# Kernel optimization log

Hardware: AMD Instinct MI355X
Metric: run time of the kernel (lower is better)

The kernel has to match this reference:

```python
import jax, jax.numpy as jnp
import numpy as np

B, S, D, H = 8, 1024, 1024, 16
DH = D // H  # per-head dim = 64
SCALE = float(np.sqrt(DH))  # normalize_coeff = sqrt(dim_h_k)


def _ln(x, g, b, eps=1e-5):
    m = jnp.mean(x, axis=-1, keepdims=True)
    v = jnp.mean(jnp.square(x - m), axis=-1, keepdims=True)
    return (x - m) / jnp.sqrt(v + eps) * g + b


def setup_inputs() -> dict:
    key = jax.random.key(0)
    ks = jax.random.split(key, 12)
    w = lambda k, shape: (jax.random.normal(k, shape, dtype=jnp.float32) * 0.02)
    return {
        "X": jax.random.normal(ks[0], (B, S, D), dtype=jnp.float32),
        # stacked per-head projection weights (torch Linear: y = x @ W.T + b -> store as [H, D, DH])
        "Wq": w(ks[1], (H, D, DH)), "bq": jnp.zeros((H, DH), jnp.float32),
        "Wk": w(ks[2], (H, D, DH)), "bk": jnp.zeros((H, DH), jnp.float32),
        "Wv": w(ks[3], (H, D, DH)), "bv": jnp.zeros((H, DH), jnp.float32),
        "pre_g": jnp.ones((D,), jnp.float32), "pre_b": jnp.zeros((D,), jnp.float32),
        "post_g": jnp.ones((D,), jnp.float32), "post_b": jnp.zeros((D,), jnp.float32),
        "W1": w(ks[4], (D, 2 * D)), "b1": jnp.zeros((2 * D,), jnp.float32),
        "ln1_g": jnp.ones((2 * D,), jnp.float32), "ln1_b": jnp.zeros((2 * D,), jnp.float32),
        "W2": w(ks[5], (2 * D, D)), "b2": jnp.zeros((D,), jnp.float32),
        "ln2_g": jnp.ones((D,), jnp.float32), "ln2_b": jnp.zeros((D,), jnp.float32),
    }


def reference(X, Wq, bq, Wk, bk, Wv, bv, pre_g, pre_b, post_g, post_b,
              W1, b1, ln1_g, ln1_b, W2, b2, ln2_g, ln2_b):
    # pre-LN + multi-head attention (all heads batched instead of python loop)
    t = _ln(X, pre_g, pre_b)
    q = jnp.einsum('bsd,hdk->bhsk', t, Wq) + bq[:, None, :]   # [B,H,S,DH]
    k = jnp.einsum('bsd,hdk->bhsk', t, Wk) + bk[:, None, :]
    v = jnp.einsum('bsd,hdk->bhsk', t, Wv) + bv[:, None, :]
    scores = jnp.einsum('bhqd,bhkd->bhqk', q, k) / SCALE       # [B,H,S,S]
    p = jax.nn.softmax(scores, axis=-1)
    o = jnp.einsum('bhqk,bhkd->bhqd', p, v)                    # [B,H,S,DH]
    o = o.transpose(0, 2, 1, 3).reshape(B, S, D)               # concat heads
    X = X + o
    # post-LN + MLP (Linear -> LN -> GELU -> Linear -> LN -> GELU)
    t2 = _ln(X, post_g, post_b)
    h = jax.nn.gelu(_ln(t2 @ W1 + b1, ln1_g, ln1_b), approximate=False)
    h = jax.nn.gelu(_ln(h @ W2 + b2, ln2_g, ln2_b), approximate=False)
    return X + h
```

## Files before the change

### kernel.cpp

```cpp
#include <hip/hip_runtime.h>

typedef __attribute__((ext_vector_type(8))) short s16x8;
typedef __attribute__((ext_vector_type(8))) unsigned short u16x8;
typedef __attribute__((ext_vector_type(4))) unsigned short u16x4;
typedef __attribute__((ext_vector_type(4))) float f32x4;

__device__ __forceinline__ unsigned short f2bf(float f) {
  union { float f; unsigned int u; } v; v.f = f;
  unsigned int r = (v.u + 0x7FFFu + ((v.u >> 16) & 1u)) >> 16;
  return (unsigned short)r;
}
__device__ __forceinline__ float bf2f(unsigned short h) {
  union { unsigned int u; float f; } v; v.u = ((unsigned int)h) << 16;
  return v.f;
}
__device__ __forceinline__ float gelu(float x) {
  return 0.5f * x * (1.f + erff(x * 0.70710678118654752f));
}
__device__ __forceinline__ float fexp2(float x) {
  float r; asm("v_exp_f32 %0, %1" : "=v"(r) : "v"(x)); return r;
}

__device__ __forceinline__ void gld16(const void* g, void* l) {
  __builtin_amdgcn_global_load_lds(
      (const __attribute__((address_space(1))) unsigned int*)g,
      (__attribute__((address_space(3))) unsigned int*)l, 16, 0, 0);
}

__device__ __forceinline__ float blk_sum(float v, float* red, int tid, int nw) {
#pragma unroll
  for (int m = 32; m >= 1; m >>= 1) v += __shfl_xor(v, m);
  __syncthreads();
  if ((tid & 63) == 0) red[tid >> 6] = v;
  __syncthreads();
  float t = 0.f;
  for (int i = 0; i < nw; ++i) t += red[i];
  return t;
}

__global__ __launch_bounds__(256) void k_tr(
    const float* __restrict__ in, unsigned short* __restrict__ out,
    int inRS, int outRS, long inBS, long outBS) {
  __shared__ float t[32][33];
  const float* ip = in + (size_t)blockIdx.z * inBS;
  unsigned short* op = out + (size_t)blockIdx.z * outBS;
  const int r0 = blockIdx.y * 32, c0 = blockIdx.x * 32;
  const int tid = threadIdx.x;
  const int r = tid >> 3, c4 = (tid & 7) * 4;
  const f32x4 v = *(const f32x4*)(ip + (size_t)(r0 + r) * inRS + c0 + c4);
#pragma unroll
  for (int i = 0; i < 4; ++i) t[r][c4 + i] = v[i];
  __syncthreads();
  u16x4 o;
#pragma unroll
  for (int i = 0; i < 4; ++i) o[i] = f2bf(t[c4 + i][r]);
  *(u16x4*)(op + (size_t)(c0 + r) * outRS + r0 + c4) = o;
}

__global__ __launch_bounds__(256) void k_bias3(
    const float* __restrict__ a, const float* __restrict__ b,
    const float* __restrict__ c, float* __restrict__ o) {
  int i = blockIdx.x * 256 + threadIdx.x;
  if (i >= 3072) return;
  o[i] = (i < 1024) ? a[i] : ((i < 2048) ? b[i - 1024] : c[i - 2048]);
}

__global__ __launch_bounds__(256) void k_pre_ln(
    const float* __restrict__ X, const float* __restrict__ g,
    const float* __restrict__ bta, unsigned short* __restrict__ out) {
  __shared__ float red[4];
  const int row = blockIdx.x, tid = threadIdx.x;
  const f32x4 x = *(const f32x4*)(X + (size_t)row * 1024 + tid * 4);
  float s = x[0] + x[1] + x[2] + x[3];
  s = blk_sum(s, red, tid, 4);
  const float mean = s * (1.f / 1024.f);
  f32x4 d;
#pragma unroll
  for (int i = 0; i < 4; ++i) d[i] = x[i] - mean;
  float sq = d[0] * d[0] + d[1] * d[1] + d[2] * d[2] + d[3] * d[3];
  sq = blk_sum(sq, red, tid, 4);
  const float rstd = rsqrtf(sq * (1.f / 1024.f) + 1e-5f);
  const f32x4 gv = *(const f32x4*)(g + tid * 4);
  const f32x4 bv = *(const f32x4*)(bta + tid * 4);
  u16x4 o;
#pragma unroll
  for (int i = 0; i < 4; ++i) o[i] = f2bf(d[i] * rstd * gv[i] + bv[i]);
  *(u16x4*)(out + (size_t)row * 1024 + tid * 4) = o;
}

__global__ __launch_bounds__(256) void k_res_ln(
    const float* __restrict__ X, const unsigned short* __restrict__ attn,
    const float* __restrict__ g, const float* __restrict__ bta,
    float* __restrict__ X1, unsigned short* __restrict__ t2) {
  __shared__ float red[4];
  const int row = blockIdx.x, tid = threadIdx.x;
  const f32x4 x = *(const f32x4*)(X + (size_t)row * 1024 + tid * 4);
  const u16x4 a = *(const u16x4*)(attn + (size_t)row * 1024 + tid * 4);
  f32x4 x1;
#pragma unroll
  for (int i = 0; i < 4; ++i) x1[i] = x[i] + bf2f(a[i]);
  *(f32x4*)(X1 + (size_t)row * 1024 + tid * 4) = x1;
  float s = x1[0] + x1[1] + x1[2] + x1[3];
  s = blk_sum(s, red, tid, 4);
  const float mean = s * (1.f / 1024.f);
  f32x4 d;
#pragma unroll
  for (int i = 0; i < 4; ++i) d[i] = x1[i] - mean;
  float sq = d[0] * d[0] + d[1] * d[1] + d[2] * d[2] + d[3] * d[3];
  sq = blk_sum(sq, red, tid, 4);
  const float rstd = rsqrtf(sq * (1.f / 1024.f) + 1e-5f);
  const f32x4 gv = *(const f32x4*)(g + tid * 4);
  const f32x4 bv = *(const f32x4*)(bta + tid * 4);
  u16x4 o;
#pragma unroll
  for (int i = 0; i < 4; ++i) o[i] = f2bf(d[i] * rstd * gv[i] + bv[i]);
  *(u16x4*)(t2 + (size_t)row * 1024 + tid * 4) = o;
}

__global__ __launch_bounds__(256) void k_ln_gelu(
    const unsigned short* __restrict__ in, const float* __restrict__ g,
    const float* __restrict__ bta, unsigned short* __restrict__ out) {
  __shared__ float red[4];
  const int row = blockIdx.x, tid = threadIdx.x;
  const u16x8 iv = *(const u16x8*)(in + (size_t)row * 2048 + tid * 8);
  float v[8];
  float s = 0.f;
#pragma unroll
  for (int i = 0; i < 8; ++i) { v[i] = bf2f(iv[i]); s += v[i]; }
  s = blk_sum(s, red, tid, 4);
  const float mean = s * (1.f / 2048.f);
  float sq = 0.f;
#pragma unroll
  for (int i = 0; i < 8; ++i) { v[i] -= mean; sq += v[i] * v[i]; }
  sq = blk_sum(sq, red, tid, 4);
  const float rstd = rsqrtf(sq * (1.f / 2048.f) + 1e-5f);
  u16x8 o;
#pragma unroll
  for (int i = 0; i < 8; ++i) {
    float t = v[i] * rstd * g[tid * 8 + i] + bta[tid * 8 + i];
    o[i] = f2bf(gelu(t));
  }
  *(u16x8*)(out + (size_t)row * 2048 + tid * 8) = o;
}

__global__ __launch_bounds__(256) void k_final(
    const unsigned short* __restrict__ in, const float* __restrict__ g,
    const float* __restrict__ bta, float* __restrict__ io) {
  __shared__ float red[4];
  const int row = blockIdx.x, tid = threadIdx.x;
  const u16x4 iv = *(const u16x4*)(in + (size_t)row * 1024 + tid * 4);
  float v[4];
  float s = 0.f;
#pragma unroll
  for (int i = 0; i < 4; ++i) { v[i] = bf2f(iv[i]); s += v[i]; }
  s = blk_sum(s, red, tid, 4);
  const float mean = s * (1.f / 1024.f);
  float sq = 0.f;
#pragma unroll
  for (int i = 0; i < 4; ++i) { v[i] -= mean; sq += v[i] * v[i]; }
  sq = blk_sum(sq, red, tid, 4);
  const float rstd = rsqrtf(sq * (1.f / 1024.f) + 1e-5f);
  const f32x4 gv = *(const f32x4*)(g + tid * 4);
  const f32x4 bv = *(const f32x4*)(bta + tid * 4);
  f32x4 xi = *(const f32x4*)(io + (size_t)row * 1024 + tid * 4);
#pragma unroll
  for (int i = 0; i < 4; ++i)
    xi[i] += gelu(v[i] * rstd * gv[i] + bv[i]);
  *(f32x4*)(io + (size_t)row * 1024 + tid * 4) = xi;
}

__global__ __launch_bounds__(256) void k_gemm3(
    const unsigned short* __restrict__ A, const unsigned short* __restrict__ Bt,
    const float* __restrict__ bias, unsigned short* __restrict__ C,
    int M, int N, int K, int vsplit, unsigned short* __restrict__ VtO) {
  __shared__ __align__(16) unsigned short lds[2][16384];
  const int tid = threadIdx.x;
  const int w = tid >> 6, l = tid & 63;
  const int wm = w >> 1, wn = w & 1;
  const int gx = gridDim.x;
  int flat = blockIdx.y * gx + blockIdx.x;
  const int nwg = gx * gridDim.y;
  flat = (flat & 7) * (nwg >> 3) + (flat >> 3);
  const int m0 = (flat / gx) * 128, n0 = (flat % gx) * 128;

  const f32x4 z4 = {0.f, 0.f, 0.f, 0.f};
  f32x4 acc[4][4];
#pragma unroll
  for (int i = 0; i < 4; ++i)
#pragma unroll
    for (int j = 0; j < 4; ++j) acc[i][j] = z4;

#define STG(t, d)                                                                   \
  {                                                                                 \
    const int kb = (t) * 64;                                                        \
    _Pragma("unroll") for (int i = 0; i < 4; ++i) {                                 \
      const int s = i * 256 + tid;                                                  \
      const int row = s >> 3, cs = s & 7;                                           \
      gld16(A + (size_t)(m0 + row) * K + kb + ((cs ^ (row & 7)) << 3),              \
            &lds[d][s * 8]);                                                        \
    }                                                                               \
    _Pragma("unroll") for (int i = 0; i < 4; ++i) {                                 \
      const int s = i * 256 + tid;                                                  \
      const int row = s >> 3, cs = s & 7;                                           \
      gld16(Bt + (size_t)(n0 + row) * K + kb + ((cs ^ (row & 7)) << 3),             \
            &lds[d][8192 + s * 8]);                                                 \
    }                                                                               \
  }

  const int nt = K >> 6;
  STG(0, 0);
  for (int t = 0; t < nt; ++t) {
    const int cur = t & 1;
    if (t + 1 < nt) {
      STG(t + 1, cur ^ 1);
      asm volatile("s_waitcnt vmcnt(8)" ::: "memory");
    } else {
      asm volatile("s_waitcnt vmcnt(0)" ::: "memory");
    }
    __builtin_amdgcn_s_barrier();
    asm volatile("" ::: "memory");
    __builtin_amdgcn_s_setprio(1);
#pragma unroll
    for (int ks = 0; ks < 2; ++ks) {
      const int g = ks * 4 + (l >> 4);
      s16x8 a[4], b[4];
#pragma unroll
      for (int m = 0; m < 4; ++m) {
        const int row = wm * 64 + m * 16 + (l & 15);
        a[m] = *(const s16x8*)&lds[cur][row * 64 + ((g ^ (row & 7)) << 3)];
      }
#pragma unroll
      for (int n = 0; n < 4; ++n) {
        const int row = wn * 64 + n * 16 + (l & 15);
        b[n] = *(const s16x8*)&lds[cur][8192 + row * 64 + ((g ^ (row & 7)) << 3)];
      }
#pragma unroll
      for (int m = 0; m < 4; ++m)
#pragma unroll
        for (int n = 0; n < 4; ++n)
          acc[m][n] = __builtin_amdgcn_mfma_f32_16x16x32_bf16(a[m], b[n], acc[m][n], 0, 0, 0);
    }
    __builtin_amdgcn_s_setprio(0);
    asm volatile("s_waitcnt lgkmcnt(0)" ::: "memory");
    __builtin_amdgcn_s_barrier();
    asm volatile("" ::: "memory");
  }
#undef STG

  const int rbase = m0 + wm * 64 + ((l >> 4) << 2);
  const int cbase = n0 + wn * 64 + (l & 15);
#pragma unroll
  for (int n = 0; n < 4; ++n) {
    const int c = cbase + n * 16;
    const float bb = bias[c];
    if ((n0 + wn * 64 + n * 16) < vsplit) {
#pragma unroll
      for (int m = 0; m < 4; ++m)
#pragma unroll
        for (int r = 0; r < 4; ++r)
          C[(size_t)(rbase + m * 16 + r) * N + c] = f2bf(acc[m][n][r] + bb);
    } else {
      const int cc = c - vsplit;
      const int hh = cc >> 6, dd = cc & 63;
#pragma unroll
      for (int m = 0; m < 4; ++m) {
        const int rr = rbase + m * 16;
        u16x4 o;
#pragma unroll
        for (int r = 0; r < 4; ++r) o[r] = f2bf(acc[m][n][r] + bb);
        *(u16x4*)(VtO + ((size_t)((rr >> 10) * 16 + hh)) * 65536 + dd * 1024 + (rr & 1023)) = o;
      }
    }
  }
}

__device__ __forceinline__ int swz(int r, int c) {
  return r * 64 + (c ^ ((r & 7) << 3));
}

__global__ __launch_bounds__(256) void k_attn3(
    const unsigned short* __restrict__ qkv, const unsigned short* __restrict__ Vt,
    unsigned short* __restrict__ O) {
  int bid = blockIdx.x;
  bid = (bid & 7) * 256 + (bid >> 3);
  const int qt = bid & 15, h = (bid >> 4) & 15, b = bid >> 8;
  const int tid = threadIdx.x, w = tid >> 6, l = tid & 63;
  const int arow = l & 15, kcol = (l >> 4) * 8;

  __shared__ __align__(16) unsigned short Kb[2][64 * 64];
  __shared__ __align__(16) unsigned short Vb[2][64 * 64];
  __shared__ __align__(16) unsigned short Ps[4][16 * 64];
  unsigned short* ps = &Ps[w][0];

  const unsigned short* qb = qkv + (size_t)b * 1024 * 3072 + h * 64;
  const unsigned short* kb = qb + 1024;
  const unsigned short* vt = Vt + ((size_t)(b * 16 + h)) * 65536;
  const int q0 = qt * 64 + w * 16;

  const float c2 = 0.125f * 1.44269504088896f;

  s16x8 qa[2];
#pragma unroll
  for (int kh = 0; kh < 2; ++kh) {
    s16x8 q = *(const s16x8*)(qb + (size_t)(q0 + arow) * 3072 + kh * 32 + kcol);
#pragma unroll
    for (int j = 0; j < 8; ++j)
      q[j] = (short)f2bf(bf2f((unsigned short)q[j]) * c2);
    qa[kh] = q;
  }
  s16x8 ones;
#pragma unroll
  for (int j = 0; j < 8; ++j) ones[j] = (short)0x3F80;

  const int srow = tid >> 3;
  const int sce = 8 * ((tid & 7) ^ (srow & 7));
  const int sdst = srow * 64 + (tid & 7) * 8;

#pragma unroll
  for (int i = 0; i < 2; ++i) {
    gld16(kb + (size_t)(i * 32 + srow) * 3072 + sce, Kb[0] + i * 2048 + sdst);
    gld16(vt + (size_t)(i * 32 + srow) * 1024 + sce, Vb[0] + i * 2048 + sdst);
  }
  __syncthreads();

  const f32x4 z4 = {0.f, 0.f, 0.f, 0.f};
  f32x4 oacc[4];
#pragma unroll
  for (int i = 0; i < 4; ++i) oacc[i] = z4;
  f32x4 lacc = z4;
  float mrun[4];
#pragma unroll
  for (int r = 0; r < 4; ++r) mrun[r] = -1e30f;

  for (int kc = 0; kc < 16; ++kc) {
    const int cur = kc & 1;
    if (kc < 15) {
      const int key1 = (kc + 1) * 64;
#pragma unroll
      for (int i = 0; i < 2; ++i) {
        gld16(kb + (size_t)(key1 + i * 32 + srow) * 3072 + sce, Kb[cur ^ 1] + i * 2048 + sdst);
        gld16(vt + (size_t)(i * 32 + srow) * 1024 + key1 + sce, Vb[cur ^ 1] + i * 2048 + sdst);
      }
    }
    f32x4 sacc[4];
#pragma unroll
    for (int t = 0; t < 4; ++t) {
      s16x8 k0 = *(const s16x8*)(Kb[cur] + swz(t * 16 + arow, kcol));
      s16x8 k1 = *(const s16x8*)(Kb[cur] + swz(t * 16 + arow, 32 + kcol));
      f32x4 s = z4;
      s = __builtin_amdgcn_mfma_f32_16x16x32_bf16(qa[0], k0, s, 0, 0, 0);
      s = __builtin_amdgcn_mfma_f32_16x16x32_bf16(qa[1], k1, s, 0, 0, 0);
      sacc[t] = s;
    }
    float rmax[4];
#pragma unroll
    for (int r = 0; r < 4; ++r) {
      float m = fmaxf(fmaxf(sacc[0][r], sacc[1][r]), fmaxf(sacc[2][r], sacc[3][r]));
#pragma unroll
      for (int msk = 8; msk >= 1; msk >>= 1) m = fmaxf(m, __shfl_xor(m, msk));
      rmax[r] = m;
    }
    const float need = fmaxf(fmaxf(rmax[0] - mrun[0], rmax[1] - mrun[1]),
                             fmaxf(rmax[2] - mrun[2], rmax[3] - mrun[3]));
    if (!__all(need <= 8.f)) {
      float sc[4];
#pragma unroll
      for (int r = 0; r < 4; ++r) {
        const float nm = fmaxf(mrun[r], rmax[r]);
        sc[r] = fexp2(mrun[r] - nm);
        mrun[r] = nm;
      }
#pragma unroll
      for (int r = 0; r < 4; ++r) {
        lacc[r] *= sc[r];
#pragma unroll
        for (int dg = 0; dg < 4; ++dg) oacc[dg][r] *= sc[r];
      }
    }
#pragma unroll
    for (int t = 0; t < 4; ++t)
#pragma unroll
      for (int r = 0; r < 4; ++r) {
        const float p = fexp2(sacc[t][r] - mrun[r]);
        ps[swz(((l >> 4) << 2) + r, t * 16 + arow)] = f2bf(p);
      }
    s16x8 pa[2];
#pragma unroll
    for (int kh = 0; kh < 2; ++kh)
      pa[kh] = *(const s16x8*)(ps + swz(arow, kh * 32 + kcol));
    lacc = __builtin_amdgcn_mfma_f32_16x16x32_bf16(pa[0], ones, lacc, 0, 0, 0);
    lacc = __builtin_amdgcn_mfma_f32_16x16x32_bf16(pa[1], ones, lacc, 0, 0, 0);
#pragma unroll
    for (int dg = 0; dg < 4; ++dg) {
      s16x8 v0 = *(const s16x8*)(Vb[cur] + swz(dg * 16 + arow, kcol));
      s16x8 v1 = *(const s16x8*)(Vb[cur] + swz(dg * 16 + arow, 32 + kcol));
      oacc[dg] = __builtin_amdgcn_mfma_f32_16x16x32_bf16(pa[0], v0, oacc[dg], 0, 0, 0);
      oacc[dg] = __builtin_amdgcn_mfma_f32_16x16x32_bf16(pa[1], v1, oacc[dg], 0, 0, 0);
    }
    __syncthreads();
  }

  float inv[4];
#pragma unroll
  for (int r = 0; r < 4; ++r) inv[r] = 1.f / lacc[r];
#pragma unroll
  for (int dg = 0; dg < 4; ++dg)
#pragma unroll
    for (int r = 0; r < 4; ++r) {
      const int row = q0 + ((l >> 4) << 2) + r;
      O[(size_t)(b * 1024 + row) * 1024 + h * 64 + dg * 16 + arow] = f2bf(oacc[dg][r] * inv[r]);
    }
}

extern "C" void kernel_launch(void* const* d_in, const int* in_sizes, int n_in,
                              void* d_out, int out_size, void* d_ws, size_t ws_size,
                              hipStream_t stream) {
  const float* X = (const float*)d_in[0];
  const float* Wq = (const float*)d_in[1];
  const float* bq = (const float*)d_in[2];
  const float* Wk = (const float*)d_in[3];
  const float* bk = (const float*)d_in[4];
  const float* Wv = (const float*)d_in[5];
  const float* bv = (const float*)d_in[6];
  const float* pre_g = (const float*)d_in[7];
  const float* pre_b = (const float*)d_in[8];
  const float* post_g = (const float*)d_in[9];
  const float* post_b = (const float*)d_in[10];
  const float* W1 = (const float*)d_in[11];
  const float* b1 = (const float*)d_in[12];
  const float* ln1_g = (const float*)d_in[13];
  const float* ln1_b = (const float*)d_in[14];
  const float* W2 = (const float*)d_in[15];
  const float* b2 = (const float*)d_in[16];
  const float* ln2_g = (const float*)d_in[17];
  const float* ln2_b = (const float*)d_in[18];
  float* out = (float*)d_out;

  char* ws = (char*)d_ws;
  const size_t MB = (size_t)1 << 20;
  unsigned short* t_bf = (unsigned short*)(ws);
  unsigned short* attn_o = (unsigned short*)(ws);
  unsigned short* mlp2 = (unsigned short*)(ws);
  unsigned short* qkv = (unsigned short*)(ws + 16 * MB);
  unsigned short* mlp1 = (unsigned short*)(ws + 16 * MB);
  unsigned short* Vt = (unsigned short*)(ws + 64 * MB);
  unsigned short* h1 = (unsigned short*)(ws + 48 * MB);
  unsigned short* t2 = (unsigned short*)(ws + 80 * MB);
  unsigned short* Wqkvt = (unsigned short*)(ws + 96 * MB);
  unsigned short* W1t = (unsigned short*)(ws + 102 * MB);
  unsigned short* W2t = (unsigned short*)(ws + 106 * MB);
  float* biasq = (float*)(ws + 110 * MB);

  k_tr<<<dim3(2, 32, 16), 256, 0, stream>>>(Wq, Wqkvt, 64, 1024, 65536, 65536);
  k_tr<<<dim3(2, 32, 16), 256, 0, stream>>>(Wk, Wqkvt + 1048576, 64, 1024, 65536, 65536);
  k_tr<<<dim3(2, 32, 16), 256, 0, stream>>>(Wv, Wqkvt + 2097152, 64, 1024, 65536, 65536);
  k_tr<<<dim3(64, 32, 1), 256, 0, stream>>>(W1, W1t, 2048, 1024, 0, 0);
  k_tr<<<dim3(32, 64, 1), 256, 0, stream>>>(W2, W2t, 1024, 2048, 0, 0);
  k_bias3<<<12, 256, 0, stream>>>(bq, bk, bv, biasq);

  k_pre_ln<<<8192, 256, 0, stream>>>(X, pre_g, pre_b, t_bf);
  k_gemm3<<<dim3(24, 64), 256, 0, stream>>>(t_bf, Wqkvt, biasq, qkv, 8192, 3072, 1024, 2048, Vt);
  k_attn3<<<2048, 256, 0, stream>>>(qkv, Vt, attn_o);
  k_res_ln<<<8192, 256, 0, stream>>>(X, attn_o, post_g, post_b, out, t2);
  k_gemm3<<<dim3(16, 64), 256, 0, stream>>>(t2, W1t, b1, mlp1, 8192, 2048, 1024, 1 << 30, nullptr);
  k_ln_gelu<<<8192, 256, 0, stream>>>(mlp1, ln1_g, ln1_b, h1);
  k_gemm3<<<dim3(8, 64), 256, 0, stream>>>(h1, W2t, b2, mlp2, 8192, 1024, 2048, 1 << 30, nullptr);
  k_final<<<8192, 256, 0, stream>>>(mlp2, ln2_g, ln2_b, out);
}
```

Before: 468.3 us.

## Transpose attention MFMA operands so each lane owns one query row

Swaps the A/B operands of the QK^T, row-sum and PV MFMAs, so each lane holds all scores for a single query row. The softmax max then needs only two cross-lane shuffles instead of sixteen, and the running max and rescale become scalars per lane. P is packed with v_cvt_pk_bf16_f32 and written to LDS as 8-byte stores. The output goes through LDS so it can be written with coalesced 16-byte global stores. The attention math is unchanged, but the LDS store patterns and bank behaviour are different.

```diff
diff --git a/kernel.cpp b/kernel.cpp
--- a/kernel.cpp
+++ b/kernel.cpp
@@ -4,6 +4,7 @@
 typedef __attribute__((ext_vector_type(8))) unsigned short u16x8;
 typedef __attribute__((ext_vector_type(4))) unsigned short u16x4;
 typedef __attribute__((ext_vector_type(4))) float f32x4;
+typedef __attribute__((ext_vector_type(2))) unsigned int u32x2;
 
 __device__ __forceinline__ unsigned short f2bf(float f) {
   union { float f; unsigned int u; } v; v.f = f;
@@ -19,6 +20,11 @@
 }
 __device__ __forceinline__ float fexp2(float x) {
   float r; asm("v_exp_f32 %0, %1" : "=v"(r) : "v"(x)); return r;
+}
+__device__ __forceinline__ unsigned int cvtpk(float lo, float hi) {
+  unsigned int r;
+  asm("v_cvt_pk_bf16_f32 %0, %1, %2" : "=v"(r) : "v"(lo), "v"(hi));
+  return r;
 }
 
 __device__ __forceinline__ void gld16(const void* g, void* l) {
@@ -278,14 +284,14 @@
   return r * 64 + (c ^ ((r & 7) << 3));
 }
 
-__global__ __launch_bounds__(256) void k_attn3(
+__global__ __launch_bounds__(256) void k_attn4(
     const unsigned short* __restrict__ qkv, const unsigned short* __restrict__ Vt,
     unsigned short* __restrict__ O) {
   int bid = blockIdx.x;
   bid = (bid & 7) * 256 + (bid >> 3);
   const int qt = bid & 15, h = (bid >> 4) & 15, b = bid >> 8;
   const int tid = threadIdx.x, w = tid >> 6, l = tid & 63;
-  const int arow = l & 15, kcol = (l >> 4) * 8;
+  const int arow = l & 15, g = l >> 4, kcol = g * 8;
 
   __shared__ __align__(16) unsigned short Kb[2][64 * 64];
   __shared__ __align__(16) unsigned short Vb[2][64 * 64];
@@ -328,9 +334,7 @@
 #pragma unroll
   for (int i = 0; i < 4; ++i) oacc[i] = z4;
   f32x4 lacc = z4;
-  float mrun[4];
-#pragma unroll
-  for (int r = 0; r < 4; ++r) mrun[r] = -1e30f;
+  float mrun = -1e30f;
 
   for (int kc = 0; kc < 16; ++kc) {
     const int cur = kc & 1;
@@ -342,74 +346,70 @@
         gld16(vt + (size_t)(i * 32 + srow) * 1024 + key1 + sce, Vb[cur ^ 1] + i * 2048 + sdst);
       }
     }
-    f32x4 sacc[4];
+    f32x4 st[4];
 #pragma unroll
     for (int t = 0; t < 4; ++t) {
       s16x8 k0 = *(const s16x8*)(Kb[cur] + swz(t * 16 + arow, kcol));
       s16x8 k1 = *(const s16x8*)(Kb[cur] + swz(t * 16 + arow, 32 + kcol));
       f32x4 s = z4;
-      s = __builtin_amdgcn_mfma_f32_16x16x32_bf16(qa[0], k0, s, 0, 0, 0);
-      s = __builtin_amdgcn_mfma_f32_16x16x32_bf16(qa[1], k1, s, 0, 0, 0);
-      sacc[t] = s;
-    }
-    float rmax[4];
-#pragma unroll
-    for (int r = 0; r < 4; ++r) {
-      float m = fmaxf(fmaxf(sacc[0][r], sacc[1][r]), fmaxf(sacc[2][r], sacc[3][r]));
-#pragma unroll
-      for (int msk = 8; msk >= 1; msk >>= 1) m = fmaxf(m, __shfl_xor(m, msk));
-      rmax[r] = m;
-    }
-    const float need = fmaxf(fmaxf(rmax[0] - mrun[0], rmax[1] - mrun[1]),
-                             fmaxf(rmax[2] - mrun[2], rmax[3] - mrun[3]));
-    if (!__all(need <= 8.f)) {
-      float sc[4];
-#pragma unroll
-      for (int r = 0; r < 4; ++r) {
-        const float nm = fmaxf(mrun[r], rmax[r]);
-        sc[r] = fexp2(mrun[r] - nm);
-        mrun[r] = nm;
-      }
-#pragma unroll
-      for (int r = 0; r < 4; ++r) {
-        lacc[r] *= sc[r];
-#pragma unroll
-        for (int dg = 0; dg < 4; ++dg) oacc[dg][r] *= sc[r];
-      }
-    }
-#pragma unroll
-    for (int t = 0; t < 4; ++t)
-#pragma unroll
-      for (int r = 0; r < 4; ++r) {
-        const float p = fexp2(sacc[t][r] - mrun[r]);
-        ps[swz(((l >> 4) << 2) + r, t * 16 + arow)] = f2bf(p);
-      }
+      s = __builtin_amdgcn_mfma_f32_16x16x32_bf16(k0, qa[0], s, 0, 0, 0);
+      s = __builtin_amdgcn_mfma_f32_16x16x32_bf16(k1, qa[1], s, 0, 0, 0);
+      st[t] = s;
+    }
+    float mx = fmaxf(fmaxf(st[0][0], st[0][1]), fmaxf(st[0][2], st[0][3]));
+#pragma unroll
+    for (int t = 1; t < 4; ++t)
+      mx = fmaxf(mx, fmaxf(fmaxf(st[t][0], st[t][1]), fmaxf(st[t][2], st[t][3])));
+    mx = fmaxf(mx, __shfl_xor(mx, 16));
+    mx = fmaxf(mx, __shfl_xor(mx, 32));
+    if (!__all(mx - mrun <= 8.f)) {
+      const float nm = fmaxf(mrun, mx);
+      const float sc = fexp2(mrun - nm);
+      mrun = nm;
+#pragma unroll
+      for (int r = 0; r < 4; ++r) lacc[r] *= sc;
+#pragma unroll
+      for (int dg = 0; dg < 4; ++dg)
+#pragma unroll
+        for (int r = 0; r < 4; ++r) oacc[dg][r] *= sc;
+    }
+#pragma unroll
+    for (int t = 0; t < 4; ++t) {
+      const unsigned int d0 = cvtpk(fexp2(st[t][0] - mrun), fexp2(st[t][1] - mrun));
+      const unsigned int d1 = cvtpk(fexp2(st[t][2] - mrun), fexp2(st[t][3] - mrun));
+      u32x2 u = {d0, d1};
+      *(u32x2*)(ps + swz(arow, t * 16 + 4 * g)) = u;
+    }
     s16x8 pa[2];
 #pragma unroll
     for (int kh = 0; kh < 2; ++kh)
       pa[kh] = *(const s16x8*)(ps + swz(arow, kh * 32 + kcol));
-    lacc = __builtin_amdgcn_mfma_f32_16x16x32_bf16(pa[0], ones, lacc, 0, 0, 0);
-    lacc = __builtin_amdgcn_mfma_f32_16x16x32_bf16(pa[1], ones, lacc, 0, 0, 0);
+    lacc = __builtin_amdgcn_mfma_f32_16x16x32_bf16(ones, pa[0], lacc, 0, 0, 0);
+    lacc = __builtin_amdgcn_mfma_f32_16x16x32_bf16(ones, pa[1], lacc, 0, 0, 0);
 #pragma unroll
     for (int dg = 0; dg < 4; ++dg) {
       s16x8 v0 = *(const s16x8*)(Vb[cur] + swz(dg * 16 + arow, kcol));
       s16x8 v1 = *(const s16x8*)(Vb[cur] + swz(dg * 16 + arow, 32 + kcol));
-      oacc[dg] = __builtin_amdgcn_mfma_f32_16x16x32_bf16(pa[0], v0, oacc[dg], 0, 0, 0);
-      oacc[dg] = __builtin_amdgcn_mfma_f32_16x16x32_bf16(pa[1], v1, oacc[dg], 0, 0, 0);
+      oacc[dg] = __builtin_amdgcn_mfma_f32_16x16x32_bf16(v0, pa[0], oacc[dg], 0, 0, 0);
+      oacc[dg] = __builtin_amdgcn_mfma_f32_16x16x32_bf16(v1, pa[1], oacc[dg], 0, 0, 0);
     }
     __syncthreads();
   }
 
-  float inv[4];
-#pragma unroll
-  for (int r = 0; r < 4; ++r) inv[r] = 1.f / lacc[r];
-#pragma unroll
-  for (int dg = 0; dg < 4; ++dg)
-#pragma unroll
-    for (int r = 0; r < 4; ++r) {
-      const int row = q0 + ((l >> 4) << 2) + r;
-      O[(size_t)(b * 1024 + row) * 1024 + h * 64 + dg * 16 + arow] = f2bf(oacc[dg][r] * inv[r]);
-    }
+  const float inv = 1.f / lacc[0];
+#pragma unroll
+  for (int dg = 0; dg < 4; ++dg) {
+    const unsigned int d0 = cvtpk(oacc[dg][0] * inv, oacc[dg][1] * inv);
+    const unsigned int d1 = cvtpk(oacc[dg][2] * inv, oacc[dg][3] * inv);
+    u32x2 u = {d0, d1};
+    *(u32x2*)(ps + swz(arow, dg * 16 + 4 * g)) = u;
+  }
+  const int rq = l >> 2, dc = (l & 3) * 16;
+  u16x8 o0 = *(const u16x8*)(ps + swz(rq, dc));
+  u16x8 o1 = *(const u16x8*)(ps + swz(rq, dc + 8));
+  unsigned short* orow = O + (size_t)(b * 1024 + q0 + rq) * 1024 + h * 64 + dc;
+  *(u16x8*)(orow) = o0;
+  *(u16x8*)(orow + 8) = o1;
 }
 
 extern "C" void kernel_launch(void* const* d_in, const int* in_sizes, int n_in,
@@ -460,7 +460,7 @@
 
   k_pre_ln<<<8192, 256, 0, stream>>>(X, pre_g, pre_b, t_bf);
   k_gemm3<<<dim3(24, 64), 256, 0, stream>>>(t_bf, Wqkvt, biasq, qkv, 8192, 3072, 1024, 2048, Vt);
-  k_attn3<<<2048, 256, 0, stream>>>(qkv, Vt, attn_o);
+  k_attn4<<<2048, 256, 0, stream>>>(qkv, Vt, attn_o);
   k_res_ln<<<8192, 256, 0, stream>>>(X, attn_o, post_g, post_b, out, t2);
   k_gemm3<<<dim3(16, 64), 256, 0, stream>>>(t2, W1t, b1, mlp1, 8192, 2048, 1024, 1 << 30, nullptr);
   k_ln_gelu<<<8192, 256, 0, stream>>>(mlp1, ln1_g, ln1_b, h1);
```

Result: faster. 446.4 us (-4.7%).
